# Kernel optimization log

Hardware: AMD Instinct MI355X
Metric: run time of the kernel (lower is better)

## Reference

```python
import jax, jax.numpy as jnp
import numpy as np

N_NODES = 100000
N_EDGES = 640000
H = 128

def setup_inputs() -> dict:
    key = jax.random.key(0)
    k = jax.random.split(key, 8)
    x_src = jax.random.normal(k[0], (N_NODES, H), dtype=jnp.float32)
    x_dst = jax.random.normal(k[1], (N_NODES, H), dtype=jnp.float32)
    src_idx = jax.random.randint(k[2], (N_EDGES,), 0, N_NODES, dtype=jnp.int64)
    dst_idx = jax.random.randint(k[3], (N_EDGES,), 0, N_NODES, dtype=jnp.int64)
    # torch Linear default init: U(-1/sqrt(fan_in), 1/sqrt(fan_in)); randn*scale is fine for a numeric baseline
    W1 = jax.random.normal(k[4], (H, 2 * H), dtype=jnp.float32) * (1.0 / np.sqrt(2 * H))
    b1 = jnp.zeros((H,), dtype=jnp.float32)
    W2 = jax.random.normal(k[5], (1, H), dtype=jnp.float32) * (1.0 / np.sqrt(H))
    b2 = jnp.zeros((1,), dtype=jnp.float32)
    return {"x_src": x_src, "x_dst": x_dst, "src_idx": src_idx, "dst_idx": dst_idx,
            "W1": W1, "b1": b1, "W2": W2, "b2": b2}

def reference(x_src, x_dst, src_idx, dst_idx, W1, b1, W2, b2):
    # per-edge gather of endpoint features, concat -> [E, 2H]
    h = jnp.concatenate([x_src[src_idx], x_dst[dst_idx]], axis=1)
    h = jax.nn.relu(h @ W1.T + b1)            # [E, H]
    score = (h @ W2.T + b2)[:, 0]             # [E]
    return score
```

## Files before the change

kernel.cpp:

```cpp
#include <hip/hip_runtime.h>
#include <hip/hip_bf16.h>

typedef __bf16 bf16x8 __attribute__((ext_vector_type(8)));
typedef __bf16 bf16x4 __attribute__((ext_vector_type(4)));
typedef float  f32x4  __attribute__((ext_vector_type(4)));

#define HF 128
#define W1K 256

__global__ __launch_bounds__(256) void w1_repack(
    const float* __restrict__ W1, __bf16* __restrict__ wf)
{
    const int h    = blockIdx.x;
    const int tid  = threadIdx.x;
    const int lane = tid & 63;
    const int wid  = tid >> 6;
    const int l15  = lane & 15;
    const int lg   = lane >> 4;

    for (int f = wid; f < 32; f += 4) {
        const int mt = f >> 2;
        const int kk = f & 3;
        const float* p = W1 + h * HF + (size_t)(mt * 16 + l15) * W1K
                       + kk * 32 + lg * 8;
        f32x4 a = *reinterpret_cast<const f32x4*>(p);
        f32x4 b = *reinterpret_cast<const f32x4*>(p + 4);
        bf16x8 w8;
        #pragma unroll
        for (int i = 0; i < 4; ++i) {
            w8[i]     = (__bf16)a[i];
            w8[i + 4] = (__bf16)b[i];
        }
        *reinterpret_cast<bf16x8*>(wf + ((size_t)(h * 32 + f) * 64 + lane) * 8) = w8;
    }
}

__global__ __launch_bounds__(256, 1) void node_precompute11(
    const float* __restrict__ x_src, const float* __restrict__ x_dst,
    const __bf16* __restrict__ wf,
    __bf16* __restrict__ u, __bf16* __restrict__ v, int nNodes)
{
    __shared__ __align__(16) __bf16 wlds[2][32][64][8];
    __shared__ __align__(16) float  xlds[2][64 * HF];

    const int tid  = threadIdx.x;
    const int lane = tid & 63;
    const int wid  = tid >> 6;
    const int l15  = lane & 15;
    const int lg   = lane >> 4;

    {
        __bf16* wl = &wlds[0][0][0][0];
        for (int c = tid; c < 4096; c += 256) {
            bf16x8 w8 = *reinterpret_cast<const bf16x8*>(wf + (size_t)c * 8);
            *reinterpret_cast<bf16x8*>(wl + (size_t)c * 8) = w8;
        }
    }

    const int nth = (nNodes + 63) >> 6;
    const int T   = nth * 2;

    auto STAGE = [&](int buf, int t) {
        const int h    = t & 1;
        const int trow = t >> 1;
        const float* __restrict__ xp = h ? x_dst : x_src;
        #pragma unroll
        for (int i = 0; i < 8; ++i) {
            const int G   = i * 256 + tid;
            const int row = G >> 5;
            const int q   = G & 31;
            const int qs  = q ^ (row & 7);
            const int grow = min(trow * 64 + row, nNodes - 1);
            const float* src = xp + (size_t)grow * HF + qs * 4;
            __builtin_amdgcn_global_load_lds(
                (const __attribute__((address_space(1))) void*)src,
                (__attribute__((address_space(3))) void*)&xlds[buf][(size_t)G * 4],
                16, 0, 0);
        }
    };

    int t = blockIdx.x;
    if (t >= T) return;
    STAGE(0, t);
    __syncthreads();

    int buf = 0;
    while (t < T) {
        const int tn = t + gridDim.x;
        const bool more = (tn < T);
        if (more) STAGE(buf ^ 1, tn);

        const int h    = t & 1;
        const int trow = t >> 1;
        const int row  = wid * 16 + l15;
        const int node = trow * 64 + row;

        f32x4 acc[8];
        #pragma unroll
        for (int mt = 0; mt < 8; ++mt) acc[mt] = (f32x4){0.f, 0.f, 0.f, 0.f};

        const float* xr = &xlds[buf][(size_t)row * HF];
        #pragma unroll
        for (int kk = 0; kk < 4; ++kk) {
            const int q0 = kk * 8 + lg * 2;
            f32x4 a0 = *reinterpret_cast<const f32x4*>(xr + ((q0)     ^ (row & 7)) * 4);
            f32x4 a1 = *reinterpret_cast<const f32x4*>(xr + ((q0 + 1) ^ (row & 7)) * 4);
            bf16x8 xb;
            #pragma unroll
            for (int i = 0; i < 4; ++i) {
                xb[i]     = (__bf16)a0[i];
                xb[i + 4] = (__bf16)a1[i];
            }
            #pragma unroll
            for (int mt = 0; mt < 8; ++mt) {
                bf16x8 wa = *reinterpret_cast<const bf16x8*>(&wlds[h][mt * 4 + kk][lane][0]);
                acc[mt] = __builtin_amdgcn_mfma_f32_16x16x32_bf16(
                    wa, xb, acc[mt], 0, 0, 0);
            }
        }

        if (node < nNodes) {
            __bf16* op = (h ? v : u) + (size_t)node * HF + lg * 4;
            #pragma unroll
            for (int mt = 0; mt < 8; ++mt) {
                bf16x4 o4;
                #pragma unroll
                for (int r = 0; r < 4; ++r) o4[r] = (__bf16)acc[mt][r];
                *reinterpret_cast<bf16x4*>(op + mt * 16) = o4;
            }
        }

        if (more) {
            asm volatile("s_waitcnt vmcnt(8)" ::: "memory");
            __builtin_amdgcn_sched_barrier(0);
            __builtin_amdgcn_s_barrier();
            __builtin_amdgcn_sched_barrier(0);
        }
        buf ^= 1;
        t = tn;
    }
}

__global__ __launch_bounds__(256) void edge_score_kernel(
    const __bf16* __restrict__ u, const __bf16* __restrict__ v,
    const int* __restrict__ sidx, const int* __restrict__ didx,
    const float* __restrict__ W2, const float* __restrict__ b1,
    const float* __restrict__ b2,
    float* __restrict__ out, int nEdges)
{
    const int tid = threadIdx.x;
    const int sub = tid >> 4;
    const int l16 = tid & 15;

    const int ebase = blockIdx.x * 64 + sub;

    float w2v[8], b1v[8];
    #pragma unroll
    for (int j = 0; j < 8; ++j) {
        w2v[j] = W2[l16 * 8 + j];
        b1v[j] = b1[l16 * 8 + j];
    }
    const float b2v = b2[0];

    int e[4], si[4], di[4];
    #pragma unroll
    for (int q = 0; q < 4; ++q) {
        e[q] = ebase + q * 16;
        const int c = min(e[q], nEdges - 1);
        si[q] = sidx[c];
        di[q] = didx[c];
    }

    bf16x8 uv[4], vv[4];
    #pragma unroll
    for (int q = 0; q < 4; ++q) {
        uv[q] = *reinterpret_cast<const bf16x8*>(u + (size_t)si[q] * HF + l16 * 8);
        vv[q] = *reinterpret_cast<const bf16x8*>(v + (size_t)di[q] * HF + l16 * 8);
    }

    float s[4] = {0.f, 0.f, 0.f, 0.f};
    #pragma unroll
    for (int q = 0; q < 4; ++q)
        #pragma unroll
        for (int j = 0; j < 8; ++j)
            s[q] += fmaxf((float)uv[q][j] + (float)vv[q][j] + b1v[j], 0.f) * w2v[j];

    #pragma unroll
    for (int off = 1; off < 16; off <<= 1)
        #pragma unroll
        for (int q = 0; q < 4; ++q)
            s[q] += __shfl_xor(s[q], off, 64);

    if (l16 == 0) {
        #pragma unroll
        for (int q = 0; q < 4; ++q)
            if (e[q] < nEdges) out[e[q]] = s[q] + b2v;
    }
}

__global__ __launch_bounds__(256, 2) void edge_mlp_kernel(
    const float* __restrict__ x_src, const float* __restrict__ x_dst,
    const int*   __restrict__ src_idx, const int* __restrict__ dst_idx,
    const float* __restrict__ W1, const float* __restrict__ b1,
    const float* __restrict__ W2, const float* __restrict__ b2,
    float* __restrict__ out, int nEdges)
{
    __shared__ __align__(16) __bf16 w1lds[64 * 64 * 8];

    const int tid  = threadIdx.x;
    const int lane = tid & 63;
    const int wid  = tid >> 6;
    const int l15  = lane & 15;
    const int lg   = lane >> 4;

    for (int p = wid; p < 64; p += 4) {
        const int n   = p >> 3;
        const int kk  = p & 7;
        const float* src = W1 + (n * 16 + l15) * W1K + kk * 32 + lg * 8;
        bf16x8 w8;
        #pragma unroll
        for (int i = 0; i < 8; ++i) w8[i] = (__bf16)src[i];
        *reinterpret_cast<bf16x8*>(&w1lds[(p * 64 + lane) * 8]) = w8;
    }
    __syncthreads();

    float w2v[8], b1v[8];
    #pragma unroll
    for (int n = 0; n < 8; ++n) {
        w2v[n] = W2[n * 16 + l15];
        b1v[n] = b1[n * 16 + l15];
    }
    const float b2v = b2[0];

    const int ntiles = nEdges / 256;
    for (int t = blockIdx.x; t < ntiles; t += gridDim.x) {
        const int ebase = t * 256 + wid * 64;

        const float* srow[4];
        const float* drow[4];
        #pragma unroll
        for (int m = 0; m < 4; ++m) {
            const int e  = ebase + m * 16 + l15;
            srow[m] = x_src + (size_t)src_idx[e] * HF + lg * 8;
            drow[m] = x_dst + (size_t)dst_idx[e] * HF + lg * 8;
        }

        f32x4 acc[4][8];
        #pragma unroll
        for (int m = 0; m < 4; ++m)
            #pragma unroll
            for (int n = 0; n < 8; ++n)
                acc[m][n] = (f32x4){0.f, 0.f, 0.f, 0.f};

        #pragma unroll
        for (int kk = 0; kk < 8; ++kk) {
            bf16x8 a[4];
            #pragma unroll
            for (int m = 0; m < 4; ++m) {
                const float* p = (kk < 4) ? (srow[m] + kk * 32)
                                          : (drow[m] + (kk - 4) * 32);
                f32x4 u0 = *reinterpret_cast<const f32x4*>(p);
                f32x4 u1 = *reinterpret_cast<const f32x4*>(p + 4);
                bf16x8 av;
                #pragma unroll
                for (int i = 0; i < 4; ++i) {
                    av[i]     = (__bf16)u0[i];
                    av[i + 4] = (__bf16)u1[i];
                }
                a[m] = av;
            }
            #pragma unroll
            for (int n = 0; n < 8; ++n) {
                bf16x8 bfrag = *reinterpret_cast<const bf16x8*>(
                    &w1lds[((n * 8 + kk) * 64 + lane) * 8]);
                #pragma unroll
                for (int m = 0; m < 4; ++m) {
                    acc[m][n] = __builtin_amdgcn_mfma_f32_16x16x32_bf16(
                        a[m], bfrag, acc[m][n], 0, 0, 0);
                }
            }
        }

        #pragma unroll
        for (int m = 0; m < 4; ++m) {
            float part[4];
            #pragma unroll
            for (int r = 0; r < 4; ++r) {
                float s = 0.f;
                #pragma unroll
                for (int n = 0; n < 8; ++n) {
                    float hv = acc[m][n][r] + b1v[n];
                    s += fmaxf(hv, 0.f) * w2v[n];
                }
                part[r] = s;
            }
            #pragma unroll
            for (int off = 1; off < 16; off <<= 1) {
                #pragma unroll
                for (int r = 0; r < 4; ++r)
                    part[r] += __shfl_xor(part[r], off, 64);
            }
            if (l15 == m) {
                f32x4 v4 = { part[0] + b2v, part[1] + b2v,
                             part[2] + b2v, part[3] + b2v };
                *reinterpret_cast<f32x4*>(&out[ebase + m * 16 + lg * 4]) = v4;
            }
        }
    }
}

extern "C" void kernel_launch(void* const* d_in, const int* in_sizes, int n_in,
                              void* d_out, int out_size, void* d_ws, size_t ws_size,
                              hipStream_t stream) {
    const float* x_src  = (const float*)d_in[0];
    const float* x_dst  = (const float*)d_in[1];
    const int*   sidx   = (const int*)d_in[2];
    const int*   didx   = (const int*)d_in[3];
    const float* W1     = (const float*)d_in[4];
    const float* b1     = (const float*)d_in[5];
    const float* W2     = (const float*)d_in[6];
    const float* b2     = (const float*)d_in[7];
    float* out = (float*)d_out;

    const int nEdges = in_sizes[2];
    const int nNodes = in_sizes[0] / HF;

    const size_t uvsz   = (size_t)2 * nNodes * HF;
    const size_t needed = uvsz * sizeof(__bf16) + 64 * 1024;
    if (ws_size >= needed) {
        __bf16* u  = (__bf16*)d_ws;
        __bf16* v  = u + (size_t)nNodes * HF;
        __bf16* wf = u + uvsz;

        w1_repack<<<2, 256, 0, stream>>>(W1, wf);

        node_precompute11<<<256, 256, 0, stream>>>(
            x_src, x_dst, wf, u, v, nNodes);

        const int egrid = (nEdges + 63) / 64;
        edge_score_kernel<<<egrid, 256, 0, stream>>>(
            u, v, sidx, didx, W2, b1, b2, out, nEdges);
    } else {
        edge_mlp_kernel<<<512, 256, 0, stream>>>(
            x_src, x_dst, sidx, didx, W1, b1, W2, b2, out, nEdges);
    }
}
```

Baseline: 88.21 us.

## Make node precompute wave-independent with register-held W1 and double edges per block

The node projection kernel now uses 512-thread blocks in which each wave owns its own 16-node slab and its own double-buffered LDS stage. Each wave keeps its half of the bf16 W1 fragments in registers instead of LDS, and replaces the block-wide barrier with per-wave vmcnt waits. The edge scoring kernel now handles eight edges per 16-lane group instead of four, putting more gathers in flight per thread. The fast path now requires nNodes divisible by 16, and the 32 register-held fragments raise register pressure.

```diff
diff --git a/kernel.cpp b/kernel.cpp
--- a/kernel.cpp
+++ b/kernel.cpp
@@ -35,13 +35,12 @@
     }
 }
 
-__global__ __launch_bounds__(256, 1) void node_precompute11(
+__global__ __launch_bounds__(512, 1) void node_precompute13(
     const float* __restrict__ x_src, const float* __restrict__ x_dst,
     const __bf16* __restrict__ wf,
     __bf16* __restrict__ u, __bf16* __restrict__ v, int nNodes)
 {
-    __shared__ __align__(16) __bf16 wlds[2][32][64][8];
-    __shared__ __align__(16) float  xlds[2][64 * HF];
+    __shared__ __align__(16) float xlds[8][2][2048];
 
     const int tid  = threadIdx.x;
     const int lane = tid & 63;
@@ -49,62 +48,65 @@
     const int l15  = lane & 15;
     const int lg   = lane >> 4;
 
+    const int h = wid & 1;
+    const float* __restrict__ xh = h ? x_dst : x_src;
+    __bf16* __restrict__ oph = h ? v : u;
+
+    bf16x8 wfrag[32];
     {
-        __bf16* wl = &wlds[0][0][0][0];
-        for (int c = tid; c < 4096; c += 256) {
-            bf16x8 w8 = *reinterpret_cast<const bf16x8*>(wf + (size_t)c * 8);
-            *reinterpret_cast<bf16x8*>(wl + (size_t)c * 8) = w8;
-        }
-    }
-
-    const int nth = (nNodes + 63) >> 6;
-    const int T   = nth * 2;
-
-    auto STAGE = [&](int buf, int t) {
-        const int h    = t & 1;
-        const int trow = t >> 1;
-        const float* __restrict__ xp = h ? x_dst : x_src;
+        const __bf16* wsrc = wf + ((size_t)h * 32 * 64 + lane) * 8;
+        #pragma unroll
+        for (int f = 0; f < 32; ++f)
+            wfrag[f] = *reinterpret_cast<const bf16x8*>(wsrc + (size_t)f * 64 * 8);
+    }
+
+    const int nst    = nNodes >> 4;
+    const int stride = gridDim.x * 4;
+
+    auto STAGE = [&](int buf, int st) {
         #pragma unroll
         for (int i = 0; i < 8; ++i) {
-            const int G   = i * 256 + tid;
+            const int G   = i * 64 + lane;
             const int row = G >> 5;
             const int q   = G & 31;
             const int qs  = q ^ (row & 7);
-            const int grow = min(trow * 64 + row, nNodes - 1);
-            const float* src = xp + (size_t)grow * HF + qs * 4;
+            const int grow = min(st * 16 + row, nNodes - 1);
+            const float* src = xh + (size_t)grow * HF + qs * 4;
             __builtin_amdgcn_global_load_lds(
                 (const __attribute__((address_space(1))) void*)src,
-                (__attribute__((address_space(3))) void*)&xlds[buf][(size_t)G * 4],
+                (__attribute__((address_space(3))) void*)&xlds[wid][buf][(size_t)G * 4],
                 16, 0, 0);
         }
     };
 
-    int t = blockIdx.x;
-    if (t >= T) return;
-    STAGE(0, t);
-    __syncthreads();
+    int st = blockIdx.x * 4 + (wid >> 1);
+    if (st >= nst) return;
+    STAGE(0, st);
+    asm volatile("s_waitcnt vmcnt(0)" ::: "memory");
+    __builtin_amdgcn_sched_barrier(0);
 
     int buf = 0;
-    while (t < T) {
-        const int tn = t + gridDim.x;
-        const bool more = (tn < T);
-        if (more) STAGE(buf ^ 1, tn);
-
-        const int h    = t & 1;
-        const int trow = t >> 1;
-        const int row  = wid * 16 + l15;
-        const int node = trow * 64 + row;
+    while (st < nst) {
+        const int stn = st + stride;
+        const bool more = (stn < nst);
+        if (more) {
+            STAGE(buf ^ 1, stn);
+            asm volatile("s_waitcnt vmcnt(16)" ::: "memory");
+        } else {
+            asm volatile("s_waitcnt vmcnt(8)" ::: "memory");
+        }
+        __builtin_amdgcn_sched_barrier(0);
 
         f32x4 acc[8];
         #pragma unroll
         for (int mt = 0; mt < 8; ++mt) acc[mt] = (f32x4){0.f, 0.f, 0.f, 0.f};
 
-        const float* xr = &xlds[buf][(size_t)row * HF];
+        const float* xr = &xlds[wid][buf][(size_t)l15 * 128];
         #pragma unroll
         for (int kk = 0; kk < 4; ++kk) {
             const int q0 = kk * 8 + lg * 2;
-            f32x4 a0 = *reinterpret_cast<const f32x4*>(xr + ((q0)     ^ (row & 7)) * 4);
-            f32x4 a1 = *reinterpret_cast<const f32x4*>(xr + ((q0 + 1) ^ (row & 7)) * 4);
+            f32x4 a0 = *reinterpret_cast<const f32x4*>(xr + ((q0)     ^ (l15 & 7)) * 4);
+            f32x4 a1 = *reinterpret_cast<const f32x4*>(xr + ((q0 + 1) ^ (l15 & 7)) * 4);
             bf16x8 xb;
             #pragma unroll
             for (int i = 0; i < 4; ++i) {
@@ -112,15 +114,14 @@
                 xb[i + 4] = (__bf16)a1[i];
             }
             #pragma unroll
-            for (int mt = 0; mt < 8; ++mt) {
-                bf16x8 wa = *reinterpret_cast<const bf16x8*>(&wlds[h][mt * 4 + kk][lane][0]);
+            for (int mt = 0; mt < 8; ++mt)
                 acc[mt] = __builtin_amdgcn_mfma_f32_16x16x32_bf16(
-                    wa, xb, acc[mt], 0, 0, 0);
-            }
-        }
-
-        if (node < nNodes) {
-            __bf16* op = (h ? v : u) + (size_t)node * HF + lg * 4;
+                    wfrag[mt * 4 + kk], xb, acc[mt], 0, 0, 0);
+        }
+
+        {
+            const int node = st * 16 + l15;
+            __bf16* op = oph + (size_t)node * HF + lg * 4;
             #pragma unroll
             for (int mt = 0; mt < 8; ++mt) {
                 bf16x4 o4;
@@ -130,14 +131,8 @@
             }
         }
 
-        if (more) {
-            asm volatile("s_waitcnt vmcnt(8)" ::: "memory");
-            __builtin_amdgcn_sched_barrier(0);
-            __builtin_amdgcn_s_barrier();
-            __builtin_amdgcn_sched_barrier(0);
-        }
         buf ^= 1;
-        t = tn;
+        st = stn;
     }
 }
 
@@ -152,7 +147,7 @@
     const int sub = tid >> 4;
     const int l16 = tid & 15;
 
-    const int ebase = blockIdx.x * 64 + sub;
+    const int ebase = blockIdx.x * 128 + sub;
 
     float w2v[8], b1v[8];
     #pragma unroll
@@ -162,38 +157,41 @@
     }
     const float b2v = b2[0];
 
-    int e[4], si[4], di[4];
-    #pragma unroll
-    for (int q = 0; q < 4; ++q) {
+    int e[8], si[8], di[8];
+    #pragma unroll
+    for (int q = 0; q < 8; ++q) {
         e[q] = ebase + q * 16;
         const int c = min(e[q], nEdges - 1);
         si[q] = sidx[c];
         di[q] = didx[c];
     }
 
-    bf16x8 uv[4], vv[4];
-    #pragma unroll
-    for (int q = 0; q < 4; ++q) {
+    bf16x8 uv[8], vv[8];
+    #pragma unroll
+    for (int q = 0; q < 8; ++q) {
         uv[q] = *reinterpret_cast<const bf16x8*>(u + (size_t)si[q] * HF + l16 * 8);
         vv[q] = *reinterpret_cast<const bf16x8*>(v + (size_t)di[q] * HF + l16 * 8);
     }
 
-    float s[4] = {0.f, 0.f, 0.f, 0.f};
-    #pragma unroll
-    for (int q = 0; q < 4; ++q)
+    float s[8];
+    #pragma unroll
+    for (int q = 0; q < 8; ++q) {
+        float acc = 0.f;
         #pragma unroll
         for (int j = 0; j < 8; ++j)
-            s[q] += fmaxf((float)uv[q][j] + (float)vv[q][j] + b1v[j], 0.f) * w2v[j];
+            acc += fmaxf((float)uv[q][j] + (float)vv[q][j] + b1v[j], 0.f) * w2v[j];
+        s[q] = acc;
+    }
 
     #pragma unroll
     for (int off = 1; off < 16; off <<= 1)
         #pragma unroll
-        for (int q = 0; q < 4; ++q)
+        for (int q = 0; q < 8; ++q)
             s[q] += __shfl_xor(s[q], off, 64);
 
     if (l16 == 0) {
         #pragma unroll
-        for (int q = 0; q < 4; ++q)
+        for (int q = 0; q < 8; ++q)
             if (e[q] < nEdges) out[e[q]] = s[q] + b2v;
     }
 }
@@ -327,17 +325,17 @@
 
     const size_t uvsz   = (size_t)2 * nNodes * HF;
     const size_t needed = uvsz * sizeof(__bf16) + 64 * 1024;
-    if (ws_size >= needed) {
+    if (ws_size >= needed && (nNodes & 15) == 0) {
         __bf16* u  = (__bf16*)d_ws;
         __bf16* v  = u + (size_t)nNodes * HF;
         __bf16* wf = u + uvsz;
 
         w1_repack<<<2, 256, 0, stream>>>(W1, wf);
 
-        node_precompute11<<<256, 256, 0, stream>>>(
+        node_precompute13<<<256, 512, 0, stream>>>(
             x_src, x_dst, wf, u, v, nNodes);
 
-        const int egrid = (nEdges + 63) / 64;
+        const int egrid = (nEdges + 127) / 128;
         edge_score_kernel<<<egrid, 256, 0, stream>>>(
             u, v, sidx, didx, W2, b1, b2, out, nEdges);
     } else {
```

New measurement: 82.22 us. 6.8% less time.
